# Kernel tuning notes

Hardware: AMD Instinct MI355X
Metric: run time of the kernel (lower is better)

The kernel has to match this reference:

```python
import jax, jax.numpy as jnp
import numpy as np

NUM_HEADS = 16
ROPE_BASE = 10000.0


def _rope_interleaved(x, cos, sin):
    # x: [B,S,H,Hd]; cos/sin: [S,Hd/2]. Interleaved pairs (even, odd).
    x1 = x[..., 0::2]
    x2 = x[..., 1::2]
    c = cos[None, :, None, :]
    s = sin[None, :, None, :]
    o1 = x1 * c - x2 * s
    o2 = x1 * s + x2 * c
    return jnp.stack([o1, o2], axis=-1).reshape(x.shape)


def setup_inputs() -> dict:
    key = jax.random.key(0)
    ks = jax.random.split(key, 5)
    B, S, D = 2, 2048, 2048
    init_scale = 0.02
    x = jax.random.normal(ks[0], (B, S, D), jnp.float32)
    Wq = jax.random.normal(ks[1], (D, D), jnp.float32) * init_scale
    Wk = jax.random.normal(ks[2], (D, D), jnp.float32) * init_scale
    Wv = jax.random.normal(ks[3], (D, D), jnp.float32) * init_scale
    Wo = jax.random.normal(ks[4], (D, D), jnp.float32) * init_scale
    return {"x": x, "Wq": Wq, "Wk": Wk, "Wv": Wv, "Wo": Wo}


def reference(x, Wq, Wk, Wv, Wo):
    B, S, D = x.shape
    H = NUM_HEADS
    Hd = D // H
    # QKV projections (bias-free)
    q = (x @ Wq).reshape(B, S, H, Hd)
    k = (x @ Wk).reshape(B, S, H, Hd)
    v = (x @ Wv).reshape(B, S, H, Hd)
    # Rotary embedding, interleaved, base 10000, full head_dim
    pos = jnp.arange(S, dtype=jnp.float32)
    inv_freq = 1.0 / (ROPE_BASE ** (jnp.arange(0, Hd, 2, dtype=jnp.float32) / Hd))
    angles = pos[:, None] * inv_freq[None, :]  # [S, Hd/2]
    cos, sin = jnp.cos(angles), jnp.sin(angles)
    q = _rope_interleaved(q, cos, sin)
    k = _rope_interleaved(k, cos, sin)
    # Causal scaled-dot-product attention (flash_attn_func default scale = Hd**-0.5)
    scale = Hd ** -0.5
    scores = jnp.einsum('bqhd,bkhd->bhqk', q, k) * scale
    causal = jnp.tril(jnp.ones((S, S), dtype=bool))
    scores = jnp.where(causal[None, None], scores, jnp.finfo(scores.dtype).min)
    probs = jax.nn.softmax(scores, axis=-1)
    attn = jnp.einsum('bhqk,bkhd->bqhd', probs, v).reshape(B, S, D)
    return attn @ Wo
```

## Files before the change

kernel.cpp:

```cpp
#include <hip/hip_runtime.h>
#include <hip/hip_bf16.h>

static constexpr int BB = 2;
static constexpr int SS = 2048;
static constexpr int DD = 2048;
static constexpr int HH = 16;
static constexpr int HD = 128;

typedef __bf16 bf16_t;
typedef __bf16 bf16x8 __attribute__((ext_vector_type(8)));
typedef __bf16 bf16x4 __attribute__((ext_vector_type(4)));
typedef float  floatx4 __attribute__((ext_vector_type(4)));

__device__ __forceinline__ void gl2lds16(const bf16_t* g, bf16_t* l) {
    __builtin_amdgcn_global_load_lds(
        (const __attribute__((address_space(1))) void*)g,
        (__attribute__((address_space(3))) void*)l, 16, 0, 0);
}

__global__ void cast_x_kernel(const float* __restrict__ x, bf16_t* __restrict__ xb) {
    int i = blockIdx.x * 256 + threadIdx.x;
    float4 v = ((const float4*)x)[i];
    bf16x4 o;
    o.x = (bf16_t)v.x; o.y = (bf16_t)v.y; o.z = (bf16_t)v.z; o.w = (bf16_t)v.w;
    ((bf16x4*)xb)[i] = o;
}

__global__ void transpose_cast_kernel(const float* __restrict__ W, bf16_t* __restrict__ Wt) {
    __shared__ float tile[32][33];
    int bx = blockIdx.x * 32;
    int by = blockIdx.y * 32;
    int tx = threadIdx.x, ty = threadIdx.y;
#pragma unroll
    for (int j = 0; j < 4; ++j)
        tile[ty + j * 8][tx] = W[(size_t)(by + ty + j * 8) * DD + bx + tx];
    __syncthreads();
#pragma unroll
    for (int j = 0; j < 4; ++j)
        Wt[(size_t)(bx + ty + j * 8) * DD + by + tx] = (bf16_t)tile[tx][ty + j * 8];
}

template <int MODE>
__global__ __launch_bounds__(256, 2) void gemm_bt_kernel(
    const bf16_t* __restrict__ A, const bf16_t* __restrict__ Bt,
    float* __restrict__ Cf, bf16_t* __restrict__ Qw, bf16_t* __restrict__ Kw,
    bf16_t* __restrict__ Vtw, int N, int K) {
    __shared__ __align__(16) bf16_t As[128 * 64];
    __shared__ __align__(16) bf16_t Bs[128 * 64];

    const int t = threadIdx.x;
    const int lane = t & 63;
    const int wave = t >> 6;
    const int lrow = lane & 15;
    const int lkq  = lane >> 4;
    const int wm = (wave & 1) * 64;
    const int wn = (wave >> 1) * 64;
    const int m0 = blockIdx.y * 128;
    const int n0 = blockIdx.x * 128;

    floatx4 acc[4][4];
#pragma unroll
    for (int i = 0; i < 4; ++i)
#pragma unroll
        for (int j = 0; j < 4; ++j) acc[i][j] = (floatx4)0.0f;

    const int srow  = lane >> 3;
    const int sch   = (lane & 7) ^ srow;
    const int swoff = (lane & 7) ^ (lrow & 7);

    for (int k0 = 0; k0 < K; k0 += 64) {
        __syncthreads();
#pragma unroll
        for (int p = 0; p < 4; ++p) {
            int r = wave * 32 + p * 8 + srow;
            gl2lds16(A  + (size_t)(m0 + r) * K + k0 + sch * 8, As + (wave * 32 + p * 8) * 64);
            gl2lds16(Bt + (size_t)(n0 + r) * K + k0 + sch * 8, Bs + (wave * 32 + p * 8) * 64);
        }
        __syncthreads();
#pragma unroll
        for (int ks = 0; ks < 2; ++ks) {
            bf16x8 af[4], bg[4];
#pragma unroll
            for (int i = 0; i < 4; ++i) {
                int pos = ((ks * 4 + lkq) ^ (lrow & 7)) * 8;
                af[i] = *(const bf16x8*)(As + (wm + i * 16 + lrow) * 64 + pos);
                bg[i] = *(const bf16x8*)(Bs + (wn + i * 16 + lrow) * 64 + pos);
            }
#pragma unroll
            for (int i = 0; i < 4; ++i)
#pragma unroll
                for (int j = 0; j < 4; ++j)
                    acc[i][j] = __builtin_amdgcn_mfma_f32_16x16x32_bf16(af[i], bg[j], acc[i][j], 0, 0, 0);
        }
    }
    (void)swoff;

#pragma unroll
    for (int i = 0; i < 4; ++i)
#pragma unroll
        for (int j = 0; j < 4; ++j)
#pragma unroll
            for (int r = 0; r < 4; ++r) {
                int m = m0 + wm + i * 16 + lkq * 4 + r;
                int n = n0 + wn + j * 16 + lrow;
                float v = acc[i][j][r];
                if (MODE == 1) {
                    Cf[(size_t)m * N + n] = v;
                } else {
                    bf16_t bv = (bf16_t)v;
                    int b = m >> 11, s = m & (SS - 1);
                    if (n < DD) {
                        int h = n >> 7, d = n & 127;
                        Qw[(((size_t)b * HH + h) * SS + s) * HD + d] = bv;
                    } else if (n < 2 * DD) {
                        int nn = n - DD;
                        int h = nn >> 7, d = nn & 127;
                        Kw[(((size_t)b * HH + h) * SS + s) * HD + d] = bv;
                    } else {
                        int nn = n - 2 * DD;
                        int h = nn >> 7, d = nn & 127;
                        Vtw[(((size_t)b * HH + h) * HD + d) * SS + s] = bv;
                    }
                }
            }
}

__global__ void rope_kernel(bf16_t* __restrict__ Qw, bf16_t* __restrict__ Kw) {
    int idx = blockIdx.x * 256 + threadIdx.x;
    int i  = idx & 63;
    int s  = (idx >> 6) & (SS - 1);
    int bh = idx >> 17;
    float inv = expf(-(float)(2 * i) * (9.210340371976184f / 128.0f));
    float ang = (float)s * inv;
    float c = cosf(ang), sn = sinf(ang);
    size_t base = ((size_t)bh * SS + s) * HD + 2 * i;
    float q1 = (float)Qw[base], q2 = (float)Qw[base + 1];
    Qw[base]     = (bf16_t)(q1 * c - q2 * sn);
    Qw[base + 1] = (bf16_t)(q1 * sn + q2 * c);
    float k1 = (float)Kw[base], k2 = (float)Kw[base + 1];
    Kw[base]     = (bf16_t)(k1 * c - k2 * sn);
    Kw[base + 1] = (bf16_t)(k1 * sn + k2 * c);
}

__global__ __launch_bounds__(256, 3) void flash_attn_kernel(
    const bf16_t* __restrict__ Qw, const bf16_t* __restrict__ Kw,
    const bf16_t* __restrict__ Vtw, bf16_t* __restrict__ Attn) {
    __shared__ __align__(16) bf16_t Ks[64 * 128];
    __shared__ __align__(16) bf16_t Vs[128 * 64];
    __shared__ __align__(16) bf16_t Ps[4][16 * 72];

    const int t = threadIdx.x;
    const int lane = t & 63;
    const int wave = t >> 6;
    const int lrow = lane & 15;
    const int lkq  = lane >> 4;
    const int bx = blockIdx.x;
    const int qtile = (bx & 1) ? (bx >> 1) : (31 - (bx >> 1));
    const int bh = blockIdx.y;
    const int q0 = qtile * 64;

    const bf16_t* Qbh = Qw + (size_t)bh * SS * HD;
    const bf16_t* Kbh = Kw + (size_t)bh * SS * HD;
    const bf16_t* Vbh = Vtw + (size_t)bh * HD * SS;

    const float qscale = 0.08838834764831845f * 1.4426950408889634f;
    bf16x8 qf[4];
#pragma unroll
    for (int kc4 = 0; kc4 < 4; ++kc4) {
        qf[kc4] = *(const bf16x8*)(Qbh + (size_t)(q0 + wave * 16 + lrow) * HD + kc4 * 32 + lkq * 8);
#pragma unroll
        for (int e = 0; e < 8; ++e) qf[kc4][e] = (bf16_t)((float)qf[kc4][e] * qscale);
    }

    floatx4 oacc[8];
#pragma unroll
    for (int i = 0; i < 8; ++i) oacc[i] = (floatx4)0.0f;
    float m_i = -1e30f, l_i = 0.0f;

    const int qg = q0 + wave * 16 + lrow;

    for (int kc = 0; kc <= qtile; ++kc) {
        __syncthreads();
#pragma unroll
        for (int p = 0; p < 4; ++p) {
            int row = wave * 16 + p * 4 + (lane >> 4);
            int gch = (lane & 15) ^ (row & 7);
            gl2lds16(Kbh + (size_t)(kc * 64 + row) * HD + gch * 8,
                     Ks + (wave * 16 + p * 4) * 128);
        }
#pragma unroll
        for (int p = 0; p < 4; ++p) {
            int row = wave * 32 + p * 8 + (lane >> 3);
            int gch = (lane & 7) ^ (row & 7);
            gl2lds16(Vbh + (size_t)row * SS + kc * 64 + gch * 8,
                     Vs + (wave * 32 + p * 8) * 64);
        }
        __syncthreads();

        floatx4 sacc[4];
#pragma unroll
        for (int i = 0; i < 4; ++i) sacc[i] = (floatx4)0.0f;
#pragma unroll
        for (int nf = 0; nf < 4; ++nf)
#pragma unroll
            for (int kc4 = 0; kc4 < 4; ++kc4) {
                bf16x8 kf = *(const bf16x8*)(Ks + (nf * 16 + lrow) * 128 +
                                             (((kc4 * 4 + lkq) ^ (lrow & 7)) * 8));
                sacc[nf] = __builtin_amdgcn_mfma_f32_16x16x32_bf16(kf, qf[kc4], sacc[nf], 0, 0, 0);
            }

        float mx = m_i;
#pragma unroll
        for (int nf = 0; nf < 4; ++nf)
#pragma unroll
            for (int r = 0; r < 4; ++r) {
                int kg = kc * 64 + nf * 16 + lkq * 4 + r;
                float sv = (kg > qg) ? -1e30f : sacc[nf][r];
                sacc[nf][r] = sv;
                mx = fmaxf(mx, sv);
            }
        mx = fmaxf(mx, __shfl_xor(mx, 16));
        mx = fmaxf(mx, __shfl_xor(mx, 32));
        float alpha = exp2f(m_i - mx);
        m_i = mx;

        float rs = 0.0f;
#pragma unroll
        for (int nf = 0; nf < 4; ++nf)
#pragma unroll
            for (int r = 0; r < 4; ++r) {
                float pv = exp2f(sacc[nf][r] - mx);
                sacc[nf][r] = pv;
                rs += pv;
            }
        rs += __shfl_xor(rs, 16);
        rs += __shfl_xor(rs, 32);
        l_i = l_i * alpha + rs;

        float av[4];
#pragma unroll
        for (int r = 0; r < 4; ++r) av[r] = __shfl(alpha, lkq * 4 + r);
#pragma unroll
        for (int nf8 = 0; nf8 < 8; ++nf8)
#pragma unroll
            for (int r = 0; r < 4; ++r) oacc[nf8][r] *= av[r];

#pragma unroll
        for (int nf = 0; nf < 4; ++nf) {
            bf16x4 pk;
#pragma unroll
            for (int r = 0; r < 4; ++r) pk[r] = (bf16_t)sacc[nf][r];
            *(bf16x4*)(Ps[wave] + lrow * 72 + nf * 16 + lkq * 4) = pk;
        }

        bf16x8 pa[2];
#pragma unroll
        for (int k2 = 0; k2 < 2; ++k2)
            pa[k2] = *(const bf16x8*)(Ps[wave] + lrow * 72 + k2 * 32 + lkq * 8);
#pragma unroll
        for (int nf8 = 0; nf8 < 8; ++nf8)
#pragma unroll
            for (int k2 = 0; k2 < 2; ++k2) {
                bf16x8 vb = *(const bf16x8*)(Vs + (nf8 * 16 + lrow) * 64 +
                                             (((k2 * 4 + lkq) ^ (lrow & 7)) * 8));
                oacc[nf8] = __builtin_amdgcn_mfma_f32_16x16x32_bf16(pa[k2], vb, oacc[nf8], 0, 0, 0);
            }
    }

    int bb = bh >> 4, h = bh & 15;
#pragma unroll
    for (int r = 0; r < 4; ++r) {
        float invl = 1.0f / __shfl(l_i, lkq * 4 + r);
        int q = q0 + wave * 16 + lkq * 4 + r;
#pragma unroll
        for (int nf8 = 0; nf8 < 8; ++nf8)
            Attn[((size_t)bb * SS + q) * DD + h * HD + nf8 * 16 + lrow] =
                (bf16_t)(oacc[nf8][r] * invl);
    }
}

extern "C" void kernel_launch(void* const* d_in, const int* in_sizes, int n_in,
                              void* d_out, int out_size, void* d_ws, size_t ws_size,
                              hipStream_t stream) {
    const float* x  = (const float*)d_in[0];
    const float* Wq = (const float*)d_in[1];
    const float* Wk = (const float*)d_in[2];
    const float* Wv = (const float*)d_in[3];
    const float* Wo = (const float*)d_in[4];
    float* out = (float*)d_out;

    bf16_t* p = (bf16_t*)d_ws;
    bf16_t* Xb    = p; p += (size_t)BB * SS * DD;
    bf16_t* Wqkvt = p; p += (size_t)3 * DD * DD;
    bf16_t* Wot   = p; p += (size_t)DD * DD;
    bf16_t* Qw    = p; p += (size_t)BB * HH * SS * HD;
    bf16_t* Kw    = p; p += (size_t)BB * HH * SS * HD;
    bf16_t* Vtw   = p; p += (size_t)BB * HH * SS * HD;
    bf16_t* Attn  = p; p += (size_t)BB * SS * DD;

    cast_x_kernel<<<(BB * SS * DD / 4) / 256, 256, 0, stream>>>(x, Xb);

    dim3 tb(32, 8), tg(DD / 32, DD / 32);
    transpose_cast_kernel<<<tg, tb, 0, stream>>>(Wq, Wqkvt);
    transpose_cast_kernel<<<tg, tb, 0, stream>>>(Wk, Wqkvt + (size_t)DD * DD);
    transpose_cast_kernel<<<tg, tb, 0, stream>>>(Wv, Wqkvt + (size_t)2 * DD * DD);
    transpose_cast_kernel<<<tg, tb, 0, stream>>>(Wo, Wot);

    gemm_bt_kernel<0><<<dim3(3 * DD / 128, BB * SS / 128), 256, 0, stream>>>(
        Xb, Wqkvt, nullptr, Qw, Kw, Vtw, 3 * DD, DD);

    rope_kernel<<<(BB * HH * SS * 64) / 256, 256, 0, stream>>>(Qw, Kw);

    flash_attn_kernel<<<dim3(SS / 64, BB * HH), 256, 0, stream>>>(Qw, Kw, Vtw, Attn);

    gemm_bt_kernel<1><<<dim3(DD / 128, BB * SS / 128), 256, 0, stream>>>(
        Attn, Wot, out, nullptr, nullptr, nullptr, DD, DD);
}
```

Before: 463.4 us.

## Process 128 query rows per flash-attention block to reuse K/V tiles

Each flash-attention block now handles two 64-row query sub-tiles (128 rows total), with each wave keeping two sets of Q fragments, accumulators and softmax state. Every K/V tile loaded into LDS is reused for both sub-tiles, which halves the global-to-LDS traffic per query row and the number of barriers. The causal mask is now applied only on diagonal chunks, and fully masked sub-tiles are skipped. The cost is roughly double the accumulator registers, which may reduce occupancy under launch_bounds(256,3), and half as many blocks in the grid.

```diff
diff --git a/kernel.cpp b/kernel.cpp
--- a/kernel.cpp
+++ b/kernel.cpp
@@ -66,7 +66,6 @@
 
     const int srow  = lane >> 3;
     const int sch   = (lane & 7) ^ srow;
-    const int swoff = (lane & 7) ^ (lrow & 7);
 
     for (int k0 = 0; k0 < K; k0 += 64) {
         __syncthreads();
@@ -93,7 +92,6 @@
                     acc[i][j] = __builtin_amdgcn_mfma_f32_16x16x32_bf16(af[i], bg[j], acc[i][j], 0, 0, 0);
         }
     }
-    (void)swoff;
 
 #pragma unroll
     for (int i = 0; i < 4; ++i)
@@ -155,31 +153,37 @@
     const int lrow = lane & 15;
     const int lkq  = lane >> 4;
     const int bx = blockIdx.x;
-    const int qtile = (bx & 1) ? (bx >> 1) : (31 - (bx >> 1));
+    const int qtile = (bx & 1) ? (bx >> 1) : (15 - (bx >> 1));
     const int bh = blockIdx.y;
-    const int q0 = qtile * 64;
+    const int q0 = qtile * 128;
 
     const bf16_t* Qbh = Qw + (size_t)bh * SS * HD;
     const bf16_t* Kbh = Kw + (size_t)bh * SS * HD;
     const bf16_t* Vbh = Vtw + (size_t)bh * HD * SS;
 
+    const int qb[2] = { q0 + wave * 16, q0 + 64 + wave * 16 };
+
     const float qscale = 0.08838834764831845f * 1.4426950408889634f;
-    bf16x8 qf[4];
-#pragma unroll
-    for (int kc4 = 0; kc4 < 4; ++kc4) {
-        qf[kc4] = *(const bf16x8*)(Qbh + (size_t)(q0 + wave * 16 + lrow) * HD + kc4 * 32 + lkq * 8);
-#pragma unroll
-        for (int e = 0; e < 8; ++e) qf[kc4][e] = (bf16_t)((float)qf[kc4][e] * qscale);
-    }
-
-    floatx4 oacc[8];
-#pragma unroll
-    for (int i = 0; i < 8; ++i) oacc[i] = (floatx4)0.0f;
-    float m_i = -1e30f, l_i = 0.0f;
-
-    const int qg = q0 + wave * 16 + lrow;
-
-    for (int kc = 0; kc <= qtile; ++kc) {
+    bf16x8 qf[2][4];
+#pragma unroll
+    for (int qs = 0; qs < 2; ++qs)
+#pragma unroll
+        for (int kc4 = 0; kc4 < 4; ++kc4) {
+            qf[qs][kc4] = *(const bf16x8*)(Qbh + (size_t)(qb[qs] + lrow) * HD + kc4 * 32 + lkq * 8);
+#pragma unroll
+            for (int e = 0; e < 8; ++e) qf[qs][kc4][e] = (bf16_t)((float)qf[qs][kc4][e] * qscale);
+        }
+
+    floatx4 oacc[2][8];
+#pragma unroll
+    for (int qs = 0; qs < 2; ++qs)
+#pragma unroll
+        for (int i = 0; i < 8; ++i) oacc[qs][i] = (floatx4)0.0f;
+    float m_i[2] = { -1e30f, -1e30f };
+    float l_i[2] = { 0.0f, 0.0f };
+
+    const int nch = 2 * qtile + 2;
+    for (int kc = 0; kc < nch; ++kc) {
         __syncthreads();
 #pragma unroll
         for (int p = 0; p < 4; ++p) {
@@ -197,86 +201,102 @@
         }
         __syncthreads();
 
-        floatx4 sacc[4];
-#pragma unroll
-        for (int i = 0; i < 4; ++i) sacc[i] = (floatx4)0.0f;
-#pragma unroll
-        for (int nf = 0; nf < 4; ++nf)
-#pragma unroll
-            for (int kc4 = 0; kc4 < 4; ++kc4) {
-                bf16x8 kf = *(const bf16x8*)(Ks + (nf * 16 + lrow) * 128 +
-                                             (((kc4 * 4 + lkq) ^ (lrow & 7)) * 8));
-                sacc[nf] = __builtin_amdgcn_mfma_f32_16x16x32_bf16(kf, qf[kc4], sacc[nf], 0, 0, 0);
+#pragma unroll
+        for (int qs = 0; qs < 2; ++qs) {
+            const int qbase = qb[qs];
+            if (kc * 64 > qbase + 15) continue;
+
+            floatx4 sacc[4];
+#pragma unroll
+            for (int i = 0; i < 4; ++i) sacc[i] = (floatx4)0.0f;
+#pragma unroll
+            for (int nf = 0; nf < 4; ++nf)
+#pragma unroll
+                for (int kc4 = 0; kc4 < 4; ++kc4) {
+                    bf16x8 kf = *(const bf16x8*)(Ks + (nf * 16 + lrow) * 128 +
+                                                 (((kc4 * 4 + lkq) ^ (lrow & 7)) * 8));
+                    sacc[nf] = __builtin_amdgcn_mfma_f32_16x16x32_bf16(kf, qf[qs][kc4], sacc[nf], 0, 0, 0);
+                }
+
+            const int qg = qbase + lrow;
+            float mx = m_i[qs];
+            if (kc * 64 + 63 > qbase) {
+#pragma unroll
+                for (int nf = 0; nf < 4; ++nf)
+#pragma unroll
+                    for (int r = 0; r < 4; ++r) {
+                        int kg = kc * 64 + nf * 16 + lkq * 4 + r;
+                        float sv = (kg > qg) ? -1e30f : sacc[nf][r];
+                        sacc[nf][r] = sv;
+                        mx = fmaxf(mx, sv);
+                    }
+            } else {
+#pragma unroll
+                for (int nf = 0; nf < 4; ++nf)
+#pragma unroll
+                    for (int r = 0; r < 4; ++r) mx = fmaxf(mx, sacc[nf][r]);
             }
-
-        float mx = m_i;
-#pragma unroll
-        for (int nf = 0; nf < 4; ++nf)
-#pragma unroll
-            for (int r = 0; r < 4; ++r) {
-                int kg = kc * 64 + nf * 16 + lkq * 4 + r;
-                float sv = (kg > qg) ? -1e30f : sacc[nf][r];
-                sacc[nf][r] = sv;
-                mx = fmaxf(mx, sv);
+            mx = fmaxf(mx, __shfl_xor(mx, 16));
+            mx = fmaxf(mx, __shfl_xor(mx, 32));
+            float alpha = exp2f(m_i[qs] - mx);
+            m_i[qs] = mx;
+
+            float rs = 0.0f;
+#pragma unroll
+            for (int nf = 0; nf < 4; ++nf)
+#pragma unroll
+                for (int r = 0; r < 4; ++r) {
+                    float pv = exp2f(sacc[nf][r] - mx);
+                    sacc[nf][r] = pv;
+                    rs += pv;
+                }
+            rs += __shfl_xor(rs, 16);
+            rs += __shfl_xor(rs, 32);
+            l_i[qs] = l_i[qs] * alpha + rs;
+
+            float av[4];
+#pragma unroll
+            for (int r = 0; r < 4; ++r) av[r] = __shfl(alpha, lkq * 4 + r);
+#pragma unroll
+            for (int nf8 = 0; nf8 < 8; ++nf8)
+#pragma unroll
+                for (int r = 0; r < 4; ++r) oacc[qs][nf8][r] *= av[r];
+
+#pragma unroll
+            for (int nf = 0; nf < 4; ++nf) {
+                bf16x4 pk;
+#pragma unroll
+                for (int r = 0; r < 4; ++r) pk[r] = (bf16_t)sacc[nf][r];
+                *(bf16x4*)(Ps[wave] + lrow * 72 + nf * 16 + lkq * 4) = pk;
             }
-        mx = fmaxf(mx, __shfl_xor(mx, 16));
-        mx = fmaxf(mx, __shfl_xor(mx, 32));
-        float alpha = exp2f(m_i - mx);
-        m_i = mx;
-
-        float rs = 0.0f;
-#pragma unroll
-        for (int nf = 0; nf < 4; ++nf)
-#pragma unroll
-            for (int r = 0; r < 4; ++r) {
-                float pv = exp2f(sacc[nf][r] - mx);
-                sacc[nf][r] = pv;
-                rs += pv;
-            }
-        rs += __shfl_xor(rs, 16);
-        rs += __shfl_xor(rs, 32);
-        l_i = l_i * alpha + rs;
-
-        float av[4];
-#pragma unroll
-        for (int r = 0; r < 4; ++r) av[r] = __shfl(alpha, lkq * 4 + r);
-#pragma unroll
-        for (int nf8 = 0; nf8 < 8; ++nf8)
-#pragma unroll
-            for (int r = 0; r < 4; ++r) oacc[nf8][r] *= av[r];
-
-#pragma unroll
-        for (int nf = 0; nf < 4; ++nf) {
-            bf16x4 pk;
-#pragma unroll
-            for (int r = 0; r < 4; ++r) pk[r] = (bf16_t)sacc[nf][r];
-            *(bf16x4*)(Ps[wave] + lrow * 72 + nf * 16 + lkq * 4) = pk;
-        }
-
-        bf16x8 pa[2];
-#pragma unroll
-        for (int k2 = 0; k2 < 2; ++k2)
-            pa[k2] = *(const bf16x8*)(Ps[wave] + lrow * 72 + k2 * 32 + lkq * 8);
-#pragma unroll
-        for (int nf8 = 0; nf8 < 8; ++nf8)
-#pragma unroll
-            for (int k2 = 0; k2 < 2; ++k2) {
-                bf16x8 vb = *(const bf16x8*)(Vs + (nf8 * 16 + lrow) * 64 +
-                                             (((k2 * 4 + lkq) ^ (lrow & 7)) * 8));
-                oacc[nf8] = __builtin_amdgcn_mfma_f32_16x16x32_bf16(pa[k2], vb, oacc[nf8], 0, 0, 0);
-            }
+
+            bf16x8 pa[2];
+#pragma unroll
+            for (int k2 = 0; k2 < 2; ++k2)
+                pa[k2] = *(const bf16x8*)(Ps[wave] + lrow * 72 + k2 * 32 + lkq * 8);
+#pragma unroll
+            for (int nf8 = 0; nf8 < 8; ++nf8)
+#pragma unroll
+                for (int k2 = 0; k2 < 2; ++k2) {
+                    bf16x8 vb = *(const bf16x8*)(Vs + (nf8 * 16 + lrow) * 64 +
+                                                 (((k2 * 4 + lkq) ^ (lrow & 7)) * 8));
+                    oacc[qs][nf8] = __builtin_amdgcn_mfma_f32_16x16x32_bf16(pa[k2], vb, oacc[qs][nf8], 0, 0, 0);
+                }
+        }
     }
 
     int bb = bh >> 4, h = bh & 15;
 #pragma unroll
-    for (int r = 0; r < 4; ++r) {
-        float invl = 1.0f / __shfl(l_i, lkq * 4 + r);
-        int q = q0 + wave * 16 + lkq * 4 + r;
-#pragma unroll
-        for (int nf8 = 0; nf8 < 8; ++nf8)
-            Attn[((size_t)bb * SS + q) * DD + h * HD + nf8 * 16 + lrow] =
-                (bf16_t)(oacc[nf8][r] * invl);
-    }
+    for (int qs = 0; qs < 2; ++qs)
+#pragma unroll
+        for (int r = 0; r < 4; ++r) {
+            float invl = 1.0f / __shfl(l_i[qs], lkq * 4 + r);
+            int q = qb[qs] + lkq * 4 + r;
+#pragma unroll
+            for (int nf8 = 0; nf8 < 8; ++nf8)
+                Attn[((size_t)bb * SS + q) * DD + h * HD + nf8 * 16 + lrow] =
+                    (bf16_t)(oacc[qs][nf8][r] * invl);
+        }
 }
 
 extern "C" void kernel_launch(void* const* d_in, const int* in_sizes, int n_in,
@@ -311,7 +331,7 @@
 
     rope_kernel<<<(BB * HH * SS * 64) / 256, 256, 0, stream>>>(Qw, Kw);
 
-    flash_attn_kernel<<<dim3(SS / 64, BB * HH), 256, 0, stream>>>(Qw, Kw, Vtw, Attn);
+    flash_attn_kernel<<<dim3(SS / 128, BB * HH), 256, 0, stream>>>(Qw, Kw, Vtw, Attn);
 
     gemm_bt_kernel<1><<<dim3(DD / 128, BB * SS / 128), 256, 0, stream>>>(
         Attn, Wot, out, nullptr, nullptr, nullptr, DD, DD);
```

After: 445.5 us. 3.9% less time.
